# Kernel optimization log

Measured on AMD Instinct MI355X. Metric: run time of the kernel, lower is better.

Reference implementation:

```python
import jax, jax.numpy as jnp
import numpy as np

EPS = 1e-5

def conv1x1(h, w, b):
    # h: [B,C,H,W], w: [O,C], b: [O]
    return jnp.einsum('bchw,oc->bohw', h, w) + b[None, :, None, None]

def setup_inputs() -> dict:
    key = jax.random.key(0)
    ks = jax.random.split(key, 10)
    B, C, H, W = 4, 256, 64, 64
    x = jax.random.normal(ks[0], (B, C, H, W), dtype=jnp.float32)
    s = 0.02
    return {
        'x': x,
        'gamma': jnp.ones((C,), jnp.float32),
        'beta': jnp.zeros((C,), jnp.float32),
        'wq': jax.random.normal(ks[1], (C, C), jnp.float32) * s,
        'bq': jnp.zeros((C,), jnp.float32),
        'wk': jax.random.normal(ks[2], (C, C), jnp.float32) * s,
        'bk': jnp.zeros((C,), jnp.float32),
        'wv': jax.random.normal(ks[3], (C, C), jnp.float32) * s,
        'bv': jnp.zeros((C,), jnp.float32),
        'wp': jax.random.normal(ks[4], (C, C), jnp.float32) * s,
        'bp': jnp.zeros((C,), jnp.float32),
    }

def reference(x, gamma, beta, wq, bq, wk, bk, wv, bv, wp, bp):
    B, C, H, W = x.shape
    N = H * W
    # BatchNorm2d (training mode: batch statistics, biased variance)
    mean = jnp.mean(x, axis=(0, 2, 3))
    var = jnp.var(x, axis=(0, 2, 3))
    h = (x - mean[None, :, None, None]) * jax.lax.rsqrt(var + EPS)[None, :, None, None]
    h = h * gamma[None, :, None, None] + beta[None, :, None, None]
    q = conv1x1(h, wq, bq).reshape(B, C, N)
    k = conv1x1(h, wk, bk).reshape(B, C, N)
    v = conv1x1(h, wv, bv).reshape(B, C, N)
    # scores[b,i,j] = q_i . k_j, softmax over j (keys)
    scores = jnp.einsum('bci,bcj->bij', q, k) * (C ** -0.5)
    attn = jax.nn.softmax(scores, axis=2)
    # out[b,c,i] = sum_j attn[b,i,j] * v[b,c,j]
    out = jnp.einsum('bij,bcj->bci', attn, v).reshape(B, C, H, W)
    out = conv1x1(out, wp, bp)
    return x + out
```

## Files before the change

kernel.cpp:

```cpp
#include <hip/hip_runtime.h>
#include <cstdint>
#include <cstddef>

#define B_ 4
#define C_ 256
#define N_ 4096

typedef __attribute__((ext_vector_type(8))) short s8v;
typedef __attribute__((ext_vector_type(4))) float f4v;
typedef __attribute__((ext_vector_type(16))) float f16v;

#if defined(__has_builtin)
#if __has_builtin(__builtin_amdgcn_exp2f)
#define EXP2(x) __builtin_amdgcn_exp2f(x)
#endif
#endif
#ifndef EXP2
#define EXP2(x) exp2f(x)
#endif

#define SCHED_FENCE() __builtin_amdgcn_sched_barrier(0)

__device__ __forceinline__ unsigned short f2bf(float f) {
  unsigned int u = __builtin_bit_cast(unsigned int, f);
  return (unsigned short)((u + 0x7FFFu + ((u >> 16) & 1u)) >> 16);
}

__device__ __forceinline__ unsigned pk2bf_trunc(float lo, float hi) {
  return __builtin_amdgcn_perm(__builtin_bit_cast(unsigned, hi),
                               __builtin_bit_cast(unsigned, lo), 0x07060302u);
}

__device__ __forceinline__ f16v zf16() {
  f16v z;
#pragma unroll
  for (int i = 0; i < 16; ++i) z[i] = 0.f;
  return z;
}


__global__ __launch_bounds__(256) void bn_stats(const float* __restrict__ x,
                                                float* __restrict__ mean,
                                                float* __restrict__ rstd) {
  int c = blockIdx.x, t = threadIdx.x;
  float s = 0.f, s2 = 0.f;
  for (int b = 0; b < B_; ++b) {
    const float* p = x + ((size_t)b * C_ + c) * N_;
    for (int n = t; n < N_; n += 256) { float v = p[n]; s += v; s2 += v * v; }
  }
  __shared__ float rs[256], rs2[256];
  rs[t] = s; rs2[t] = s2; __syncthreads();
  for (int off = 128; off > 0; off >>= 1) {
    if (t < off) { rs[t] += rs[t + off]; rs2[t] += rs2[t + off]; }
    __syncthreads();
  }
  if (t == 0) {
    float m = rs[0] * (1.f / 16384.f);
    float v = rs2[0] * (1.f / 16384.f) - m * m;
    mean[c] = m; rstd[c] = rsqrtf(v + 1e-5f);
  }
}

__global__ __launch_bounds__(256) void prep(
    const float* __restrict__ wq, const float* __restrict__ bq,
    const float* __restrict__ wk, const float* __restrict__ bk,
    const float* __restrict__ wv, const float* __restrict__ bv,
    const float* __restrict__ wp,
    const float* __restrict__ gamma, const float* __restrict__ beta,
    const float* __restrict__ mean, const float* __restrict__ rstd,
    unsigned short* __restrict__ wqb, unsigned short* __restrict__ wkb,
    unsigned short* __restrict__ wvb, unsigned short* __restrict__ wpb,
    float* __restrict__ beq, float* __restrict__ bek, float* __restrict__ bev) {
  const float QSC = 0.0625f * 1.4426950408889634f;
  int o = blockIdx.x, c = threadIdx.x;
  float a = gamma[c] * rstd[c];
  float d = beta[c] - mean[c] * a;
  float wqv = wq[o * C_ + c], wkv = wk[o * C_ + c], wvv = wv[o * C_ + c];
  wqb[o * C_ + c] = f2bf(wqv * a * QSC);
  wkb[o * C_ + c] = f2bf(wkv * a);
  wvb[o * C_ + c] = f2bf(wvv * a);
  wpb[o * C_ + c] = f2bf(wp[o * C_ + c]);
  __shared__ float r0[256], r1[256], r2[256];
  r0[c] = wqv * d; r1[c] = wkv * d; r2[c] = wvv * d; __syncthreads();
  for (int off = 128; off > 0; off >>= 1) {
    if (c < off) { r0[c] += r0[c + off]; r1[c] += r1[c + off]; r2[c] += r2[c + off]; }
    __syncthreads();
  }
  if (c == 0) {
    beq[o] = (bq[o] + r0[0]) * QSC;
    bek[o] = bk[o] + r1[0];
    bev[o] = bv[o] + r2[0];
  }
}

__global__ __launch_bounds__(256) void xt(const float* __restrict__ x,
                                          unsigned short* __restrict__ xbB) {
  int b = blockIdx.z, c0 = blockIdx.y * 64, n0 = blockIdx.x * 64;
  int tid = threadIdx.x;
  __shared__ unsigned short Ls[64][72];
  int cw = tid >> 6, nl = tid & 63;
#pragma unroll
  for (int rr = 0; rr < 16; ++rr) {
    int c = c0 + cw * 16 + rr;
    Ls[nl][cw * 16 + rr] = f2bf(x[((size_t)b * C_ + c) * N_ + n0 + nl]);
  }
  __syncthreads();
  int n_ = tid >> 2, cs = (tid & 3) * 16;
  s8v v0 = *(const s8v*)(&Ls[n_][cs]);
  s8v v1 = *(const s8v*)(&Ls[n_][cs + 8]);
  int n = n0 + n_;
  size_t base = (((size_t)b * 256 + (n >> 4)) * 32 + ((c0 + cs) >> 3)) * 128 + (n & 15) * 8;
  *(s8v*)(xbB + base) = v0;
  *(s8v*)(xbB + base + 128) = v1;
}

__global__ __launch_bounds__(256) void qkv(
    const unsigned short* __restrict__ xbB,
    const unsigned short* __restrict__ wqb, const unsigned short* __restrict__ wkb,
    const unsigned short* __restrict__ wvb,
    const float* __restrict__ beq, const float* __restrict__ bek,
    const float* __restrict__ bev,
    unsigned short* __restrict__ qB, unsigned short* __restrict__ kB,
    unsigned short* __restrict__ vB) {
  int b = blockIdx.z, oblk = blockIdx.y, n0 = blockIdx.x * 64;
  int tid = threadIdx.x, w = tid >> 6, l = tid & 63, quad = l >> 4, lq = l & 15;
  int orow = oblk * 64 + w * 16 + lq;

  f4v aq[4], ak[4], av[4];
#pragma unroll
  for (int nt = 0; nt < 4; ++nt) {
    aq[nt] = (f4v){0.f, 0.f, 0.f, 0.f};
    ak[nt] = (f4v){0.f, 0.f, 0.f, 0.f};
    av[nt] = (f4v){0.f, 0.f, 0.f, 0.f};
  }

#pragma unroll
  for (int kk = 0; kk < 8; ++kk) {
    s8v afq = *(const s8v*)(wqb + (size_t)orow * C_ + kk * 32 + quad * 8);
    s8v afk = *(const s8v*)(wkb + (size_t)orow * C_ + kk * 32 + quad * 8);
    s8v afv = *(const s8v*)(wvb + (size_t)orow * C_ + kk * 32 + quad * 8);
#pragma unroll
    for (int nt = 0; nt < 4; ++nt) {
      s8v bf = *(const s8v*)(xbB + (((size_t)b * 256 + ((n0 + nt * 16) >> 4)) * 32 + kk * 4 + quad) * 128 + lq * 8);
      aq[nt] = __builtin_amdgcn_mfma_f32_16x16x32_bf16(afq, bf, aq[nt], 0, 0, 0);
      ak[nt] = __builtin_amdgcn_mfma_f32_16x16x32_bf16(afk, bf, ak[nt], 0, 0, 0);
      av[nt] = __builtin_amdgcn_mfma_f32_16x16x32_bf16(afv, bf, av[nt], 0, 0, 0);
    }
  }

  __shared__ unsigned short Ls[64][72];
  int obase = oblk * 64;

  for (int pass = 0; pass < 2; ++pass) {
    const f4v* acc = (pass == 0) ? aq : ak;
    const float* BE = (pass == 0) ? beq : bek;
    int ob4 = obase + w * 16 + quad * 4;
    float b0 = BE[ob4], b1 = BE[ob4 + 1], b2 = BE[ob4 + 2], b3 = BE[ob4 + 3];
#pragma unroll
    for (int nt = 0; nt < 4; ++nt) {
      unsigned lo = (unsigned)f2bf(acc[nt][0] + b0) | ((unsigned)f2bf(acc[nt][1] + b1) << 16);
      unsigned hi = (unsigned)f2bf(acc[nt][2] + b2) | ((unsigned)f2bf(acc[nt][3] + b3) << 16);
      uint2 pr; pr.x = lo; pr.y = hi;
      *(uint2*)(&Ls[nt * 16 + lq][w * 16 + quad * 4]) = pr;
    }
    __syncthreads();
    {
      unsigned short* dp = (pass == 0) ? qB : kB;
#pragma unroll
      for (int ii = 0; ii < 2; ++ii) {
        int i = tid + ii * 256;
        int g = i >> 8, cs = (i >> 6) & 3, ll = i & 63;
        s8v vv = *(const s8v*)(&Ls[g * 32 + (ll & 31)][cs * 16 + ((ll >> 5) << 3)]);
        size_t dst;
        if (pass == 0)
          dst = ((((size_t)b * 64 + (n0 >> 6)) * 2 + g) * 16 + (obase >> 4) + cs) * 512 + (size_t)ll * 8;
        else
          dst = (((size_t)b * 128 + (n0 >> 5) + g) * 16 + (obase >> 4) + cs) * 512 + (size_t)ll * 8;
        *(s8v*)(dp + dst) = vv;
      }
    }
    __syncthreads();
  }

#pragma unroll
  for (int nt = 0; nt < 4; ++nt)
#pragma unroll
    for (int r = 0; r < 4; ++r) {
      int o_ = obase + w * 16 + quad * 4 + r;
      Ls[w * 16 + quad * 4 + r][nt * 16 + lq] = f2bf(av[nt][r] + bev[o_]);
    }
  __syncthreads();
  {
#pragma unroll
    for (int ii = 0; ii < 2; ++ii) {
      int i = tid + ii * 256;
      int g = i >> 8, ks = (i >> 6) & 3, ll = i & 63;
      s8v vv = *(const s8v*)(&Ls[g * 32 + (ll & 31)][ks * 16 + ((ll >> 5) << 3)]);
      size_t dst = (((size_t)b * 8 + (obase >> 5) + g) * 256 + (n0 >> 4) + ks) * 512 + (size_t)ll * 8;
      *(s8v*)(vB + dst) = vv;
    }
  }
}

__global__ __launch_bounds__(512, 2) void attn(
    const unsigned short* __restrict__ qB, const unsigned short* __restrict__ kB,
    const unsigned short* __restrict__ vB, unsigned short* __restrict__ aB) {
  int id = blockIdx.x;
  int b = (id & 7) >> 1;
  int i0 = (((id >> 3) << 1) | (id & 1)) << 6;
  int tid = threadIdx.x, w = tid >> 6, l = tid & 63;
  int lh = l >> 5, l31 = l & 31;

  __shared__ unsigned short Qs[16384];
  __shared__ unsigned short Ps[2][16384];
  __shared__ float Lw[8][2][32];

  {
    const s8v* g = (const s8v*)(qB + ((size_t)b * 64 + (i0 >> 6)) * 16384);
    s8v* sq = (s8v*)Qs;
    sq[tid] = g[tid];
    sq[tid + 512] = g[tid + 512];
    sq[tid + 1024] = g[tid + 1024];
    sq[tid + 1536] = g[tid + 1536];
  }

  const unsigned short* kp = kB + (((size_t)b * 128 + w) * 16) * 512 + (size_t)l * 8;
  const unsigned short* vp = vB + (((size_t)b * 8 + w) * 256) * 512 + (size_t)l * 8;
  const unsigned short* Qp = Qs + (size_t)lh * 256 + l31 * 8;

  s8v kf[16];
#pragma unroll
  for (int cs = 0; cs < 16; ++cs) kf[cs] = *(const s8v*)(kp + cs * 512);
  SCHED_FENCE();

  __syncthreads();

  f16v O0 = zf16(), O1 = zf16();
  float ls0 = 0.f, ls1 = 0.f;

  for (int t = 0; t < 16; ++t) {
    s8v vf[16];
#pragma unroll
    for (int ks = 0; ks < 8; ++ks) vf[ks] = *(const s8v*)(vp + (size_t)ks * 512);
    SCHED_FENCE();
    f16v S0 = zf16(), S1 = zf16();
#pragma unroll
    for (int cs = 0; cs < 16; ++cs) {
      s8v q0 = *(const s8v*)(Qp + cs * 512);
      s8v q1 = *(const s8v*)(Qp + 8192 + cs * 512);
      S0 = __builtin_amdgcn_mfma_f32_32x32x16_bf16(kf[cs], q0, S0, 0, 0, 0);
      S1 = __builtin_amdgcn_mfma_f32_32x32x16_bf16(kf[cs], q1, S1, 0, 0, 0);
    }
#pragma unroll
    for (int ks = 8; ks < 16; ++ks) vf[ks] = *(const s8v*)(vp + (size_t)ks * 512);
    SCHED_FENCE();
    unsigned short* Pw = Ps[t & 1] + (w * 4) * 256 + l31 * 8 + lh * 4;
#pragma unroll
    for (int j = 0; j < 4; ++j) {
      float a0 = EXP2(S0[4 * j + 0]), a1 = EXP2(S0[4 * j + 1]);
      float a2 = EXP2(S0[4 * j + 2]), a3 = EXP2(S0[4 * j + 3]);
      ls0 += (a0 + a1) + (a2 + a3);
      uint2 p0; p0.x = pk2bf_trunc(a0, a1); p0.y = pk2bf_trunc(a2, a3);
      *(uint2*)(Pw + j * 256) = p0;
      float c0 = EXP2(S1[4 * j + 0]), c1 = EXP2(S1[4 * j + 1]);
      float c2 = EXP2(S1[4 * j + 2]), c3 = EXP2(S1[4 * j + 3]);
      ls1 += (c0 + c1) + (c2 + c3);
      uint2 p1; p1.x = pk2bf_trunc(c0, c1); p1.y = pk2bf_trunc(c2, c3);
      *(uint2*)(Pw + 8192 + j * 256) = p1;
    }
    __syncthreads();
    kp += 65536;
#pragma unroll
    for (int cs = 0; cs < 16; ++cs) kf[cs] = *(const s8v*)(kp + cs * 512);
    SCHED_FENCE();
    const unsigned short* Pr = Ps[t & 1] + (size_t)lh * 256 + l31 * 8;
#pragma unroll
    for (int ks = 0; ks < 16; ++ks) {
      s8v p0 = *(const s8v*)(Pr + ks * 512);
      s8v p1 = *(const s8v*)(Pr + 8192 + ks * 512);
      O0 = __builtin_amdgcn_mfma_f32_32x32x16_bf16(vf[ks], p0, O0, 0, 0, 0);
      O1 = __builtin_amdgcn_mfma_f32_32x32x16_bf16(vf[ks], p1, O1, 0, 0, 0);
    }
    vp += 8192;
  }

  ls0 += __shfl_xor(ls0, 32);
  ls1 += __shfl_xor(ls1, 32);
  if (l < 32) { Lw[w][0][l] = ls0; Lw[w][1][l] = ls1; }
  __syncthreads();
  float s0 = 0.f, s1 = 0.f;
#pragma unroll
  for (int ww = 0; ww < 8; ++ww) { s0 += Lw[ww][0][l31]; s1 += Lw[ww][1][l31]; }
  float rl0 = 1.f / s0, rl1 = 1.f / s1;

#pragma unroll
  for (int jj = 0; jj < 4; ++jj) {
    ushort4 pk;
    pk.x = f2bf(O0[4 * jj + 0] * rl0); pk.y = f2bf(O0[4 * jj + 1] * rl0);
    pk.z = f2bf(O0[4 * jj + 2] * rl0); pk.w = f2bf(O0[4 * jj + 3] * rl0);
    size_t ob = (((size_t)b * 256 + (i0 >> 4) + (l31 >> 4)) * 32 + w * 4 + jj) * 128
              + (l31 & 15) * 8 + lh * 4;
    *(ushort4*)(aB + ob) = pk;
    pk.x = f2bf(O1[4 * jj + 0] * rl1); pk.y = f2bf(O1[4 * jj + 1] * rl1);
    pk.z = f2bf(O1[4 * jj + 2] * rl1); pk.w = f2bf(O1[4 * jj + 3] * rl1);
    size_t ob1 = (((size_t)b * 256 + (i0 >> 4) + 2 + (l31 >> 4)) * 32 + w * 4 + jj) * 128
               + (l31 & 15) * 8 + lh * 4;
    *(ushort4*)(aB + ob1) = pk;
  }
}

__global__ __launch_bounds__(256) void proj(
    const float* __restrict__ x, const unsigned short* __restrict__ wpb,
    const float* __restrict__ bp, const unsigned short* __restrict__ aB,
    float* __restrict__ out) {
  int b = blockIdx.z, oblk = blockIdx.y, n0 = blockIdx.x * 64;
  int tid = threadIdx.x, w = tid >> 6, l = tid & 63, quad = l >> 4, lq = l & 15;
  int orow_a = oblk * 64 + w * 16 + lq;

  f4v acc[4];
#pragma unroll
  for (int nt = 0; nt < 4; ++nt) acc[nt] = (f4v){0.f, 0.f, 0.f, 0.f};

#pragma unroll
  for (int kk = 0; kk < 8; ++kk) {
    s8v af = *(const s8v*)(wpb + (size_t)orow_a * C_ + kk * 32 + quad * 8);
#pragma unroll
    for (int nt = 0; nt < 4; ++nt) {
      s8v bf = *(const s8v*)(aB + (((size_t)b * 256 + ((n0 + nt * 16) >> 4)) * 32 + kk * 4 + quad) * 128 + lq * 8);
      acc[nt] = __builtin_amdgcn_mfma_f32_16x16x32_bf16(af, bf, acc[nt], 0, 0, 0);
    }
  }
#pragma unroll
  for (int nt = 0; nt < 4; ++nt)
#pragma unroll
    for (int r = 0; r < 4; ++r) {
      int o_ = oblk * 64 + w * 16 + quad * 4 + r;
      size_t idx = ((size_t)b * C_ + o_) * N_ + n0 + nt * 16 + lq;
      out[idx] = x[idx] + acc[nt][r] + bp[o_];
    }
}

extern "C" void kernel_launch(void* const* d_in, const int* in_sizes, int n_in,
                              void* d_out, int out_size, void* d_ws, size_t ws_size,
                              hipStream_t stream) {
  const float* x     = (const float*)d_in[0];
  const float* gamma = (const float*)d_in[1];
  const float* beta  = (const float*)d_in[2];
  const float* wq    = (const float*)d_in[3];
  const float* bq    = (const float*)d_in[4];
  const float* wk    = (const float*)d_in[5];
  const float* bk    = (const float*)d_in[6];
  const float* wv    = (const float*)d_in[7];
  const float* bv    = (const float*)d_in[8];
  const float* wp    = (const float*)d_in[9];
  const float* bp    = (const float*)d_in[10];
  float* out = (float*)d_out;

  char* ws = (char*)d_ws;
  float* mean = (float*)ws; ws += 1024;
  float* rstd = (float*)ws; ws += 1024;
  float* beq  = (float*)ws; ws += 1024;
  float* bek  = (float*)ws; ws += 1024;
  float* bev  = (float*)ws; ws += 1024;
  unsigned short* wqb = (unsigned short*)ws; ws += C_ * C_ * 2;
  unsigned short* wkb = (unsigned short*)ws; ws += C_ * C_ * 2;
  unsigned short* wvb = (unsigned short*)ws; ws += C_ * C_ * 2;
  unsigned short* wpb = (unsigned short*)ws; ws += C_ * C_ * 2;
  unsigned short* xbB = (unsigned short*)ws; ws += (size_t)B_ * N_ * C_ * 2;
  unsigned short* qB  = (unsigned short*)ws; ws += (size_t)B_ * N_ * C_ * 2;
  unsigned short* kB  = (unsigned short*)ws; ws += (size_t)B_ * N_ * C_ * 2;
  unsigned short* vB  = (unsigned short*)ws; ws += (size_t)B_ * N_ * C_ * 2;
  unsigned short* aB  = (unsigned short*)ws; ws += (size_t)B_ * N_ * C_ * 2;

  hipLaunchKernelGGL(bn_stats, dim3(C_), dim3(256), 0, stream, x, mean, rstd);
  hipLaunchKernelGGL(prep, dim3(C_), dim3(256), 0, stream,
                     wq, bq, wk, bk, wv, bv, wp, gamma, beta, mean, rstd,
                     wqb, wkb, wvb, wpb, beq, bek, bev);
  hipLaunchKernelGGL(xt, dim3(N_ / 64, 4, B_), dim3(256), 0, stream, x, xbB);
  hipLaunchKernelGGL(qkv, dim3(N_ / 64, 4, B_), dim3(256), 0, stream,
                     xbB, wqb, wkb, wvb, beq, bek, bev, qB, kB, vB);
  hipLaunchKernelGGL(attn, dim3(256), dim3(512), 0, stream, qB, kB, vB, aB);
  hipLaunchKernelGGL(proj, dim3(N_ / 64, 4, B_), dim3(256), 0, stream,
                     x, wpb, bp, aB, out);
}
```

Measured before the change: 210.2 us.

## Fuse x transpose into qkv and output projection into attention kernel

Removes the standalone xt kernel by having each qkv block convert and transpose all 256 channels of its x tile into shared memory, and removes the proj kernel by doing the 1x1 output projection plus bias and residual inside the attention kernel from a shared-memory copy of the normalized attention output. This drops two launches and the xbB and aB global round trips. In exchange, each of the 4 qkv o-blocks now re-reads and re-converts x, and attn uses an extra 32KB of shared memory, which may hurt its occupancy.

```diff
diff --git a/kernel.cpp b/kernel.cpp
--- a/kernel.cpp
+++ b/kernel.cpp
@@ -93,29 +93,8 @@
   }
 }
 
-__global__ __launch_bounds__(256) void xt(const float* __restrict__ x,
-                                          unsigned short* __restrict__ xbB) {
-  int b = blockIdx.z, c0 = blockIdx.y * 64, n0 = blockIdx.x * 64;
-  int tid = threadIdx.x;
-  __shared__ unsigned short Ls[64][72];
-  int cw = tid >> 6, nl = tid & 63;
-#pragma unroll
-  for (int rr = 0; rr < 16; ++rr) {
-    int c = c0 + cw * 16 + rr;
-    Ls[nl][cw * 16 + rr] = f2bf(x[((size_t)b * C_ + c) * N_ + n0 + nl]);
-  }
-  __syncthreads();
-  int n_ = tid >> 2, cs = (tid & 3) * 16;
-  s8v v0 = *(const s8v*)(&Ls[n_][cs]);
-  s8v v1 = *(const s8v*)(&Ls[n_][cs + 8]);
-  int n = n0 + n_;
-  size_t base = (((size_t)b * 256 + (n >> 4)) * 32 + ((c0 + cs) >> 3)) * 128 + (n & 15) * 8;
-  *(s8v*)(xbB + base) = v0;
-  *(s8v*)(xbB + base + 128) = v1;
-}
-
 __global__ __launch_bounds__(256) void qkv(
-    const unsigned short* __restrict__ xbB,
+    const float* __restrict__ x,
     const unsigned short* __restrict__ wqb, const unsigned short* __restrict__ wkb,
     const unsigned short* __restrict__ wvb,
     const float* __restrict__ beq, const float* __restrict__ bek,
@@ -126,6 +105,28 @@
   int tid = threadIdx.x, w = tid >> 6, l = tid & 63, quad = l >> 4, lq = l & 15;
   int orow = oblk * 64 + w * 16 + lq;
 
+  __shared__ unsigned short XF[16384];
+  __shared__ unsigned short Ls[64][72];
+
+  {
+    int cw = tid >> 6, nl = tid & 63;
+    for (int cq = 0; cq < 4; ++cq) {
+#pragma unroll
+      for (int rr = 0; rr < 16; ++rr) {
+        int c = cq * 64 + cw * 16 + rr;
+        Ls[nl][cw * 16 + rr] = f2bf(x[((size_t)b * C_ + c) * N_ + n0 + nl]);
+      }
+      __syncthreads();
+      int n_ = tid >> 2, cs = (tid & 3) * 16;
+      s8v v0 = *(const s8v*)(&Ls[n_][cs]);
+      s8v v1 = *(const s8v*)(&Ls[n_][cs + 8]);
+      int fr = ((n_ >> 4) * 32 + ((cq * 64 + cs) >> 3)) * 128 + (n_ & 15) * 8;
+      *(s8v*)(XF + fr) = v0;
+      *(s8v*)(XF + fr + 128) = v1;
+      __syncthreads();
+    }
+  }
+
   f4v aq[4], ak[4], av[4];
 #pragma unroll
   for (int nt = 0; nt < 4; ++nt) {
@@ -141,14 +142,13 @@
     s8v afv = *(const s8v*)(wvb + (size_t)orow * C_ + kk * 32 + quad * 8);
 #pragma unroll
     for (int nt = 0; nt < 4; ++nt) {
-      s8v bf = *(const s8v*)(xbB + (((size_t)b * 256 + ((n0 + nt * 16) >> 4)) * 32 + kk * 4 + quad) * 128 + lq * 8);
+      s8v bf = *(const s8v*)(XF + (nt * 32 + kk * 4 + quad) * 128 + lq * 8);
       aq[nt] = __builtin_amdgcn_mfma_f32_16x16x32_bf16(afq, bf, aq[nt], 0, 0, 0);
       ak[nt] = __builtin_amdgcn_mfma_f32_16x16x32_bf16(afk, bf, ak[nt], 0, 0, 0);
       av[nt] = __builtin_amdgcn_mfma_f32_16x16x32_bf16(afv, bf, av[nt], 0, 0, 0);
     }
   }
 
-  __shared__ unsigned short Ls[64][72];
   int obase = oblk * 64;
 
   for (int pass = 0; pass < 2; ++pass) {
@@ -156,6 +156,7 @@
     const float* BE = (pass == 0) ? beq : bek;
     int ob4 = obase + w * 16 + quad * 4;
     float b0 = BE[ob4], b1 = BE[ob4 + 1], b2 = BE[ob4 + 2], b3 = BE[ob4 + 3];
+    __syncthreads();
 #pragma unroll
     for (int nt = 0; nt < 4; ++nt) {
       unsigned lo = (unsigned)f2bf(acc[nt][0] + b0) | ((unsigned)f2bf(acc[nt][1] + b1) << 16);
@@ -179,8 +180,8 @@
         *(s8v*)(dp + dst) = vv;
       }
     }
-    __syncthreads();
-  }
+  }
+  __syncthreads();
 
 #pragma unroll
   for (int nt = 0; nt < 4; ++nt)
@@ -204,7 +205,9 @@
 
 __global__ __launch_bounds__(512, 2) void attn(
     const unsigned short* __restrict__ qB, const unsigned short* __restrict__ kB,
-    const unsigned short* __restrict__ vB, unsigned short* __restrict__ aB) {
+    const unsigned short* __restrict__ vB,
+    const unsigned short* __restrict__ wpb, const float* __restrict__ bp,
+    const float* __restrict__ x, float* __restrict__ out) {
   int id = blockIdx.x;
   int b = (id & 7) >> 1;
   int i0 = (((id >> 3) << 1) | (id & 1)) << 6;
@@ -213,6 +216,7 @@
 
   __shared__ unsigned short Qs[16384];
   __shared__ unsigned short Ps[2][16384];
+  __shared__ unsigned short aS[16384];
   __shared__ float Lw[8][2][32];
 
   {
@@ -277,12 +281,18 @@
 #pragma unroll
     for (int ks = 0; ks < 16; ++ks) {
       s8v p0 = *(const s8v*)(Pr + ks * 512);
-      s8v p1 = *(const s8v*)(Pr + 8192 + ks * 512);
+      s8v p1 = *(const s8v*)(Pr + ks * 512 + 8192);
       O0 = __builtin_amdgcn_mfma_f32_32x32x16_bf16(vf[ks], p0, O0, 0, 0, 0);
       O1 = __builtin_amdgcn_mfma_f32_32x32x16_bf16(vf[ks], p1, O1, 0, 0, 0);
     }
     vp += 8192;
   }
+
+  s8v wf[16];
+#pragma unroll
+  for (int cs = 0; cs < 16; ++cs)
+    wf[cs] = *(const s8v*)(wpb + (size_t)(w * 32 + l31) * 256 + cs * 16 + lh * 8);
+  SCHED_FENCE();
 
   ls0 += __shfl_xor(ls0, 32);
   ls1 += __shfl_xor(ls1, 32);
@@ -298,46 +308,32 @@
     ushort4 pk;
     pk.x = f2bf(O0[4 * jj + 0] * rl0); pk.y = f2bf(O0[4 * jj + 1] * rl0);
     pk.z = f2bf(O0[4 * jj + 2] * rl0); pk.w = f2bf(O0[4 * jj + 3] * rl0);
-    size_t ob = (((size_t)b * 256 + (i0 >> 4) + (l31 >> 4)) * 32 + w * 4 + jj) * 128
-              + (l31 & 15) * 8 + lh * 4;
-    *(ushort4*)(aB + ob) = pk;
+    int f0 = ((l31 >> 4) * 32 + w * 4 + jj) * 128 + (l31 & 15) * 8 + lh * 4;
+    *(ushort4*)(aS + f0) = pk;
     pk.x = f2bf(O1[4 * jj + 0] * rl1); pk.y = f2bf(O1[4 * jj + 1] * rl1);
     pk.z = f2bf(O1[4 * jj + 2] * rl1); pk.w = f2bf(O1[4 * jj + 3] * rl1);
-    size_t ob1 = (((size_t)b * 256 + (i0 >> 4) + 2 + (l31 >> 4)) * 32 + w * 4 + jj) * 128
-               + (l31 & 15) * 8 + lh * 4;
-    *(ushort4*)(aB + ob1) = pk;
-  }
-}
-
-__global__ __launch_bounds__(256) void proj(
-    const float* __restrict__ x, const unsigned short* __restrict__ wpb,
-    const float* __restrict__ bp, const unsigned short* __restrict__ aB,
-    float* __restrict__ out) {
-  int b = blockIdx.z, oblk = blockIdx.y, n0 = blockIdx.x * 64;
-  int tid = threadIdx.x, w = tid >> 6, l = tid & 63, quad = l >> 4, lq = l & 15;
-  int orow_a = oblk * 64 + w * 16 + lq;
-
-  f4v acc[4];
-#pragma unroll
-  for (int nt = 0; nt < 4; ++nt) acc[nt] = (f4v){0.f, 0.f, 0.f, 0.f};
-
-#pragma unroll
-  for (int kk = 0; kk < 8; ++kk) {
-    s8v af = *(const s8v*)(wpb + (size_t)orow_a * C_ + kk * 32 + quad * 8);
-#pragma unroll
-    for (int nt = 0; nt < 4; ++nt) {
-      s8v bf = *(const s8v*)(aB + (((size_t)b * 256 + ((n0 + nt * 16) >> 4)) * 32 + kk * 4 + quad) * 128 + lq * 8);
-      acc[nt] = __builtin_amdgcn_mfma_f32_16x16x32_bf16(af, bf, acc[nt], 0, 0, 0);
-    }
-  }
-#pragma unroll
-  for (int nt = 0; nt < 4; ++nt)
-#pragma unroll
-    for (int r = 0; r < 4; ++r) {
-      int o_ = oblk * 64 + w * 16 + quad * 4 + r;
-      size_t idx = ((size_t)b * C_ + o_) * N_ + n0 + nt * 16 + lq;
-      out[idx] = x[idx] + acc[nt][r] + bp[o_];
-    }
+    int f1 = ((2 + (l31 >> 4)) * 32 + w * 4 + jj) * 128 + (l31 & 15) * 8 + lh * 4;
+    *(ushort4*)(aS + f1) = pk;
+  }
+  __syncthreads();
+
+  f16v OP0 = zf16(), OP1 = zf16();
+#pragma unroll
+  for (int cs = 0; cs < 16; ++cs) {
+    s8v pa0 = *(const s8v*)(aS + ((0 + (l31 >> 4)) * 32 + cs * 2 + lh) * 128 + (l31 & 15) * 8);
+    s8v pa1 = *(const s8v*)(aS + ((2 + (l31 >> 4)) * 32 + cs * 2 + lh) * 128 + (l31 & 15) * 8);
+    OP0 = __builtin_amdgcn_mfma_f32_32x32x16_bf16(wf[cs], pa0, OP0, 0, 0, 0);
+    OP1 = __builtin_amdgcn_mfma_f32_32x32x16_bf16(wf[cs], pa1, OP1, 0, 0, 0);
+  }
+
+#pragma unroll
+  for (int r = 0; r < 16; ++r) {
+    int o_ = w * 32 + (r & 3) + 8 * (r >> 2) + 4 * lh;
+    float bpv = bp[o_];
+    size_t ix = ((size_t)b * C_ + o_) * N_ + i0 + l31;
+    out[ix]      = x[ix]      + OP0[r] + bpv;
+    out[ix + 32] = x[ix + 32] + OP1[r] + bpv;
+  }
 }
 
 extern "C" void kernel_launch(void* const* d_in, const int* in_sizes, int n_in,
@@ -366,20 +362,16 @@
   unsigned short* wkb = (unsigned short*)ws; ws += C_ * C_ * 2;
   unsigned short* wvb = (unsigned short*)ws; ws += C_ * C_ * 2;
   unsigned short* wpb = (unsigned short*)ws; ws += C_ * C_ * 2;
-  unsigned short* xbB = (unsigned short*)ws; ws += (size_t)B_ * N_ * C_ * 2;
   unsigned short* qB  = (unsigned short*)ws; ws += (size_t)B_ * N_ * C_ * 2;
   unsigned short* kB  = (unsigned short*)ws; ws += (size_t)B_ * N_ * C_ * 2;
   unsigned short* vB  = (unsigned short*)ws; ws += (size_t)B_ * N_ * C_ * 2;
-  unsigned short* aB  = (unsigned short*)ws; ws += (size_t)B_ * N_ * C_ * 2;
 
   hipLaunchKernelGGL(bn_stats, dim3(C_), dim3(256), 0, stream, x, mean, rstd);
   hipLaunchKernelGGL(prep, dim3(C_), dim3(256), 0, stream,
                      wq, bq, wk, bk, wv, bv, wp, gamma, beta, mean, rstd,
                      wqb, wkb, wvb, wpb, beq, bek, bev);
-  hipLaunchKernelGGL(xt, dim3(N_ / 64, 4, B_), dim3(256), 0, stream, x, xbB);
   hipLaunchKernelGGL(qkv, dim3(N_ / 64, 4, B_), dim3(256), 0, stream,
-                     xbB, wqb, wkb, wvb, beq, bek, bev, qB, kB, vB);
-  hipLaunchKernelGGL(attn, dim3(256), dim3(512), 0, stream, qB, kB, vB, aB);
-  hipLaunchKernelGGL(proj, dim3(N_ / 64, 4, B_), dim3(256), 0, stream,
-                     x, wpb, bp, aB, out);
-}
+                     x, wqb, wkb, wvb, beq, bek, bev, qB, kB, vB);
+  hipLaunchKernelGGL(attn, dim3(256), dim3(512), 0, stream,
+                     qB, kB, vB, wpb, bp, x, out);
+}
```

Result: no change. 206.5 us (-1.7%).
